# Performance work log

Hardware: AMD Instinct MI355X
Metric: run time of the kernel (lower is better)

## Reference

```python
import jax, jax.numpy as jnp
import numpy as np

C = 64       # channels per irrep
N = 50000    # nodes
E = 800000   # edges
A = 10       # node attribute (species) dim
R = 8        # radial basis features
H = 64       # radial MLP hidden width
INV3 = 1.0 / np.sqrt(3.0)  # CG norm for 1x1->0
INV2 = 1.0 / np.sqrt(2.0)  # CG norm for 1x1->1


def setup_inputs() -> dict:
    key = jax.random.key(0)
    ks = jax.random.split(key, 20)
    rn = lambda k, s, sc=1.0: jax.random.normal(k, s, dtype=jnp.float32) * sc
    sC = 1.0 / np.sqrt(C)
    inp = {}
    inp['node_features'] = rn(ks[0], (N, 4 * C))
    inp['node_attributes'] = jax.random.uniform(ks[1], (N, A), dtype=jnp.float32)
    inp['sph_harmonics'] = rn(ks[2], (E, 4))
    inp['radial_basis'] = jax.random.uniform(ks[3], (E, R), dtype=jnp.float32)
    inp['edge_index'] = jax.random.randint(ks[4], (2, E), 0, N)
    inp['pre_W0'] = rn(ks[5], (C, C), sC)
    inp['pre_W1'] = rn(ks[6], (C, C), sC)
    inp['mlp_W1'] = rn(ks[7], (R, H), 1.0 / np.sqrt(R))
    inp['mlp_W2'] = rn(ks[8], (H, H), 1.0 / np.sqrt(H))
    inp['mlp_W3'] = rn(ks[9], (H, 5 * C), 1.0 / np.sqrt(H))
    inp['lin0'] = rn(ks[10], (C, C), sC)
    inp['lin1'] = rn(ks[11], (C, C), sC)
    inp['c0_w'] = rn(ks[12], (A, 3, C), 1.0 / np.sqrt(A))
    inp['c1_w'] = rn(ks[13], (A, 2, C), 1.0 / np.sqrt(A))
    inp['sc_W0'] = rn(ks[14], (C, A, C), sC / np.sqrt(A))
    inp['sc_W1'] = rn(ks[15], (C, A, C), sC / np.sqrt(A))
    inp['fin0'] = rn(ks[16], (C, C), sC)
    inp['fin1'] = rn(ks[17], (C, C), sC)
    return inp


def reference(node_features, node_attributes, sph_harmonics, radial_basis,
              edge_index, pre_W0, pre_W1, mlp_W1, mlp_W2, mlp_W3, lin0, lin1,
              c0_w, c1_w, sc_W0, sc_W1, fin0, fin1):
    n = node_features.shape[0]
    # split flat features into irrep blocks: scalars (0e) and vectors (1o)
    x0 = node_features[:, :C]                        # [N, C]
    x1 = node_features[:, C:].reshape(n, C, 3)       # [N, C, 3]
    # --- interaction: pre linear (per-irrep channel mixing) ---
    h0 = x0 @ pre_W0
    h1 = jnp.einsum('ncm,cd->ndm', x1, pre_W1)
    snd, rcv = edge_index[0], edge_index[1]
    n0 = h0[snd]                                     # [E, C]
    n1 = h1[snd]                                     # [E, C, 3]
    y0 = sph_harmonics[:, :1]                        # [E, 1]
    y1 = sph_harmonics[:, 1:]                        # [E, 3]
    # radial MLP -> per-edge tensor-product path weights (SiLU, no bias)
    w = jax.nn.silu(radial_basis @ mlp_W1)
    w = jax.nn.silu(w @ mlp_W2)
    w = (w @ mlp_W3).reshape(-1, 5, C)               # [E, 5 paths, C]
    # Clebsch-Gordan tensor product paths (l<=1):
    #   0x0->0, 1x1->0, 0x1->1, 1x0->1, 1x1->1 (cross product)
    m0 = w[:, 0] * n0 * y0 + w[:, 1] * INV3 * jnp.einsum('ecm,em->ec', n1, y1)
    m1 = ((w[:, 2] * n0)[:, :, None] * y1[:, None, :]
          + w[:, 3][:, :, None] * n1 * y0[:, :, None]
          + w[:, 4][:, :, None] * INV2 * jnp.cross(n1, y1[:, None, :]))
    # neighbour aggregation: sum over receivers
    t0 = jax.ops.segment_sum(m0, rcv, num_segments=n)
    t1 = jax.ops.segment_sum(m1, rcv, num_segments=n)
    # post-interaction linear
    t0 = t0 @ lin0
    t1 = jnp.einsum('ncm,cd->ndm', t1, lin1)
    # --- symmetric contraction (correlation 2), attribute-dependent weights ---
    cw0 = jnp.einsum('na,apc->npc', node_attributes, c0_w)
    cw1 = jnp.einsum('na,apc->npc', node_attributes, c1_w)
    out0 = cw0[:, 0] * t0 + cw0[:, 1] * (t0 * t0) + cw0[:, 2] * jnp.sum(t1 * t1, axis=-1)
    out1 = cw1[:, 0][:, :, None] * t1 + cw1[:, 1][:, :, None] * (t0[:, :, None] * t1)
    # --- self-connection residual (fully connected TP with attrs 0e) ---
    out0 = out0 + jnp.einsum('nc,na,cad->nd', x0, node_attributes, sc_W0)
    out1 = out1 + jnp.einsum('ncm,na,cad->ndm', x1, node_attributes, sc_W1)
    # --- final linear ---
    f0 = out0 @ fin0
    f1 = jnp.einsum('ncm,cd->ndm', out1, fin1)
    return jnp.concatenate([f0, f1.reshape(n, 3 * C)], axis=-1)
```

## Files before the change

kernel.cpp:

```cpp
#include <hip/hip_runtime.h>
#include <hip/hip_bf16.h>
#include <cstdint>
#include <cstddef>

namespace {

constexpr int kN = 50000;
constexpr int kE = 800000;
constexpr int kPl = 3200000;
constexpr float kInv3 = 0.57735026918962576451f;
constexpr float kInv2 = 0.70710678118654752440f;

typedef __attribute__((ext_vector_type(8))) short bf16x8;
typedef __attribute__((ext_vector_type(4))) float f32x4;
union FragU { uint32_t u[4]; bf16x8 v; uint4 q; };

__device__ __forceinline__ float bcast(float v, int k) {
  return __int_as_float(__builtin_amdgcn_readlane(__float_as_int(v), k));
}
__device__ __forceinline__ int bcasti(int v, int k) {
  return __builtin_amdgcn_readlane(v, k);
}
__device__ __forceinline__ float silu(float x) {
  return x / (1.0f + __expf(-x));
}
__device__ __forceinline__ uint32_t bf16r(float f) {
  uint32_t u = __float_as_uint(f);
  return (u + 0x7fffu + ((u >> 16) & 1u)) >> 16;
}
__device__ __forceinline__ float blo(uint32_t u) { return __uint_as_float(u << 16); }
__device__ __forceinline__ float bhi(uint32_t u) { return __uint_as_float(u & 0xffff0000u); }
__device__ __forceinline__ uint32_t pk(float a, float b) {
  union { __hip_bfloat16 h; unsigned short s; } x, y;
  x.h = __float2bfloat16(a);
  y.h = __float2bfloat16(b);
  return (uint32_t)x.s | ((uint32_t)y.s << 16);
}

__global__ __launch_bounds__(256) void k_pre(const float* __restrict__ nf,
                                             const float* __restrict__ W0,
                                             const float* __restrict__ W1,
                                             float4* __restrict__ hcomb,
                                             unsigned short* __restrict__ xp) {
  __shared__ float sW[8192];
  __shared__ float sbuf[4][256];
  for (int i = threadIdx.x; i < 8192; i += 256)
    sW[i] = (i < 4096) ? W0[i] : W1[i - 4096];
  __syncthreads();

  const int wid = threadIdx.x >> 6, lane = threadIdx.x & 63;
  for (int nb = blockIdx.x * 4; nb < kN; nb += 2048 * 4) {
    const int n = nb + wid;
    if (n >= kN) continue;
    const float4 rv = ((const float4*)nf)[(size_t)n * 64 + lane];
    *(float4*)&sbuf[wid][lane * 4] = rv;
    const float v0 = sbuf[wid][lane];
    const float vx = sbuf[wid][64 + 3 * lane];
    const float vy = sbuf[wid][64 + 3 * lane + 1];
    const float vz = sbuf[wid][64 + 3 * lane + 2];
    xp[(size_t)n * 64 + lane] = (unsigned short)bf16r(vx);
    xp[(size_t)kPl + (size_t)n * 64 + lane] = (unsigned short)bf16r(vy);
    xp[(size_t)2 * kPl + (size_t)n * 64 + lane] = (unsigned short)bf16r(vz);
    float a0 = 0.f, ax = 0.f, ay = 0.f, az = 0.f;
#pragma unroll
    for (int k = 0; k < 64; ++k) {
      const float w0 = sW[k * 64 + lane];
      const float w1 = sW[4096 + k * 64 + lane];
      a0 = fmaf(bcast(v0, k), w0, a0);
      ax = fmaf(bcast(vx, k), w1, ax);
      ay = fmaf(bcast(vy, k), w1, ay);
      az = fmaf(bcast(vz, k), w1, az);
    }
    hcomb[(size_t)n * 64 + lane] = make_float4(a0, ax, ay, az);
  }
}

__global__ void k_hist(const int* __restrict__ ei, int* __restrict__ cnt) {
  const int e = blockIdx.x * blockDim.x + threadIdx.x;
  if (e < kE) atomicAdd(&cnt[ei[kE + e]], 1);
}

__global__ __launch_bounds__(1024) void k_scan(const int* __restrict__ cnt,
                                               int* __restrict__ starts) {
  __shared__ int sh[1024];
  const int t = threadIdx.x;
  constexpr int CH = 49;
  const int base = t * CH;
  int s = 0;
  for (int i = 0; i < CH; ++i) {
    const int idx = base + i;
    if (idx < kN) s += cnt[idx];
  }
  sh[t] = s;
  __syncthreads();
  for (int off = 1; off < 1024; off <<= 1) {
    const int v = sh[t];
    const int o = (t >= off) ? sh[t - off] : 0;
    __syncthreads();
    sh[t] = v + o;
    __syncthreads();
  }
  int run = sh[t] - s;
  for (int i = 0; i < CH; ++i) {
    const int idx = base + i;
    if (idx < kN) {
      starts[idx] = run;
      run += cnt[idx];
    }
  }
}

__global__ void k_scatter(const int* __restrict__ ei, int* __restrict__ cursor,
                          int* __restrict__ eids) {
  const int e = blockIdx.x * blockDim.x + threadIdx.x;
  if (e < kE) {
    const int pos = atomicAdd(&cursor[ei[kE + e]], 1);
    eids[pos] = e;
  }
}

__device__ __forceinline__ void xpose(const uint32_t* pa, const uint32_t* pb,
                                      int addr0, int addr1, bool ghi,
                                      FragU* out) {
#pragma unroll
  for (int kt = 0; kt < 2; ++kt) {
    const int m0 = 2 * kt, m1 = 2 * kt + 1;
    int t0, t1;
    t0 = __builtin_amdgcn_ds_bpermute(addr0, (int)pa[m0]);
    t1 = __builtin_amdgcn_ds_bpermute(addr0, (int)pa[m1]);
    out[kt].u[0] = (uint32_t)(ghi ? t1 : t0);
    t0 = __builtin_amdgcn_ds_bpermute(addr0, (int)pb[m0]);
    t1 = __builtin_amdgcn_ds_bpermute(addr0, (int)pb[m1]);
    out[kt].u[1] = (uint32_t)(ghi ? t1 : t0);
    t0 = __builtin_amdgcn_ds_bpermute(addr1, (int)pa[m0]);
    t1 = __builtin_amdgcn_ds_bpermute(addr1, (int)pa[m1]);
    out[kt].u[2] = (uint32_t)(ghi ? t1 : t0);
    t0 = __builtin_amdgcn_ds_bpermute(addr1, (int)pb[m0]);
    t1 = __builtin_amdgcn_ds_bpermute(addr1, (int)pb[m1]);
    out[kt].u[3] = (uint32_t)(ghi ? t1 : t0);
  }
}

__global__ __launch_bounds__(256, 2) void k_mlp(
    const float* __restrict__ rb, const int* __restrict__ eids,
    const float* __restrict__ W1f, const float* __restrict__ W2f,
    const float* __restrict__ W3f, uint32_t* __restrict__ wout,
    int tile0, int ntiles) {
  __shared__ uint32_t sfrag[13312];
  for (int i = threadIdx.x; i < 13312; i += 256) {
    const int f = i >> 8, l = (i >> 2) & 63, jp = i & 3;
    const int kk = ((l >> 4) << 3) + 2 * jp;
    float a, b;
    if (f < 4) {
      const int c = (f << 4) + (l & 15);
      a = (kk < 8) ? W1f[kk * 64 + c] : 0.f;
      b = (kk < 7) ? W1f[(kk + 1) * 64 + c] : 0.f;
    } else if (f < 12) {
      const int kt = (f - 4) >> 2, mt = (f - 4) & 3;
      const int k = kt * 32 + kk, c = (mt << 4) + (l & 15);
      a = W2f[k * 64 + c];
      b = W2f[(k + 1) * 64 + c];
    } else {
      const int kt = (f - 12) / 20, mt = (f - 12) % 20;
      const int k = kt * 32 + kk, c = (mt << 4) + (l & 15);
      a = W3f[k * 320 + c];
      b = W3f[(k + 1) * 320 + c];
    }
    sfrag[i] = pk(a, b);
  }
  __syncthreads();

  const int lane = threadIdx.x & 63;
  const int e15 = lane & 15, g = lane >> 4;
  const uint4* fr = (const uint4*)sfrag;
  const int wv = blockIdx.x * 4 + (threadIdx.x >> 6);
  const int addr0 = ((((g & 1) << 1)) * 16 + e15) * 4;
  const int addr1 = addr0 + 64;
  const bool ghi = (g >> 1) != 0;
  const f32x4 z = {0.f, 0.f, 0.f, 0.f};

  for (int t = wv; t < ntiles; t += 768 * 4) {
    FragU b1;
    b1.u[0] = b1.u[1] = b1.u[2] = b1.u[3] = 0;
    if (lane < 16) {
      const int e = eids[(size_t)(tile0 + t) * 16 + lane];
      const float4 r0 = *(const float4*)(rb + (size_t)e * 8);
      const float4 r1 = *(const float4*)(rb + (size_t)e * 8 + 4);
      b1.u[0] = pk(r0.x, r0.y);
      b1.u[1] = pk(r0.z, r0.w);
      b1.u[2] = pk(r1.x, r1.y);
      b1.u[3] = pk(r1.z, r1.w);
    }

    uint32_t pa[4], pb[4];
#pragma unroll
    for (int mt = 0; mt < 4; ++mt) {
      FragU a;
      a.q = fr[(mt << 6) + lane];
      f32x4 d = __builtin_amdgcn_mfma_f32_16x16x32_bf16(a.v, b1.v, z, 0, 0, 0);
      pa[mt] = pk(silu(d[0]), silu(d[1]));
      pb[mt] = pk(silu(d[2]), silu(d[3]));
    }
    FragU b2[2];
    xpose(pa, pb, addr0, addr1, ghi, b2);

    f32x4 d2[4] = {z, z, z, z};
#pragma unroll
    for (int kt = 0; kt < 2; ++kt)
#pragma unroll
      for (int mt = 0; mt < 4; ++mt) {
        FragU a;
        a.q = fr[((4 + kt * 4 + mt) << 6) + lane];
        d2[mt] =
            __builtin_amdgcn_mfma_f32_16x16x32_bf16(a.v, b2[kt].v, d2[mt], 0, 0, 0);
      }
#pragma unroll
    for (int mt = 0; mt < 4; ++mt) {
      pa[mt] = pk(silu(d2[mt][0]), silu(d2[mt][1]));
      pb[mt] = pk(silu(d2[mt][2]), silu(d2[mt][3]));
    }
    FragU b3[2];
    xpose(pa, pb, addr0, addr1, ghi, b3);

    uint32_t* wt = wout + (size_t)t * 2560 + lane;
#pragma unroll 4
    for (int mt = 0; mt < 20; ++mt) {
      FragU a0, a1;
      a0.q = fr[((12 + mt) << 6) + lane];
      a1.q = fr[((32 + mt) << 6) + lane];
      f32x4 d = __builtin_amdgcn_mfma_f32_16x16x32_bf16(a0.v, b3[0].v, z, 0, 0, 0);
      d = __builtin_amdgcn_mfma_f32_16x16x32_bf16(a1.v, b3[1].v, d, 0, 0, 0);
      wt[mt * 128] = pk(d[0], d[1]);
      wt[mt * 128 + 64] = pk(d[2], d[3]);
    }
  }
}

__global__ __launch_bounds__(1024, 6) void k_edge2(
    const float* __restrict__ sph, const int* __restrict__ ei,
    const int* __restrict__ eids, const int* __restrict__ ends,
    const int* __restrict__ cnts, const uint32_t* __restrict__ w32,
    const float4* __restrict__ hcomb, float4* __restrict__ tcomb,
    int lo, int hi) {
  const int lane = threadIdx.x & 63;
  const int LCb = ((lane >> 4) << 7) + (((lane & 3) >> 1) << 6) +
                  (((lane >> 2) & 3) << 4);
  const uint32_t shl = (lane & 1) ? 0u : 16u;
  const int gw = blockIdx.x * 16 + (threadIdx.x >> 6);
  for (int n = gw; n < kN; n += 512 * 16) {
    int tmp = 0;
    if (lane == 0) tmp = ends[n];
    else if (lane == 1) tmp = cnts[n];
    const int end = bcasti(tmp, 0);
    const int cn = bcasti(tmp, 1);
    const int s0 = max(end - cn, lo);
    const int s1 = min(end, hi);
    if (s0 >= s1) continue;
    float a0 = 0.f, axx = 0.f, ayy = 0.f, azz = 0.f;

    for (int base = s0; base < s1; base += 64) {
      const int m = min(64, s1 - base);
      int sidv = 0;
      float4 svv = make_float4(0.f, 0.f, 0.f, 0.f);
      if (lane < m) {
        const int ev = eids[base + lane];
        sidv = ei[ev];
        svv = *(const float4*)(sph + (size_t)ev * 4);
      }
      const int scur = bcasti(sidv, 0);
      float4 h = hcomb[(size_t)scur * 64 + lane];
      const int sl0 = base - lo;
      size_t wi = (size_t)(sl0 >> 4) * 2560 + (sl0 & 15) + LCb;
      uint32_t u0 = w32[wi], u1 = w32[wi + 512], u2 = w32[wi + 1024],
               u3 = w32[wi + 1536], u4 = w32[wi + 2048];

      for (int j = 0; j < m; ++j) {
        float4 hn = h;
        uint32_t n0 = u0, n1 = u1, n2 = u2, n3 = u3, n4 = u4;
        if (j + 1 < m) {
          const int sn = bcasti(sidv, j + 1);
          hn = hcomb[(size_t)sn * 64 + lane];
          const int sl = base + j + 1 - lo;
          const size_t wj = (size_t)(sl >> 4) * 2560 + (sl & 15) + LCb;
          n0 = w32[wj];
          n1 = w32[wj + 512];
          n2 = w32[wj + 1024];
          n3 = w32[wj + 1536];
          n4 = w32[wj + 2048];
        }
        const float y0 = bcast(svv.x, j), y1 = bcast(svv.y, j);
        const float y2 = bcast(svv.z, j), y3 = bcast(svv.w, j);
        const float w0 = __uint_as_float((u0 << shl) & 0xffff0000u);
        const float w1v = __uint_as_float((u1 << shl) & 0xffff0000u);
        const float w2v = __uint_as_float((u2 << shl) & 0xffff0000u);
        const float w3v = __uint_as_float((u3 << shl) & 0xffff0000u);
        const float w4v = __uint_as_float((u4 << shl) & 0xffff0000u);

        const float dot = h.y * y1 + h.z * y2 + h.w * y3;
        const float m0 = w0 * h.x * y0 + w1v * kInv3 * dot;
        const float cx = h.z * y3 - h.w * y2;
        const float cy = h.w * y1 - h.y * y3;
        const float cz = h.y * y2 - h.z * y1;
        const float t2 = w2v * h.x;
        const float c4 = w4v * kInv2;
        const float w3y0 = w3v * y0;
        a0 += m0;
        axx += t2 * y1 + w3y0 * h.y + c4 * cx;
        ayy += t2 * y2 + w3y0 * h.z + c4 * cy;
        azz += t2 * y3 + w3y0 * h.w + c4 * cz;
        h = hn;
        u0 = n0; u1 = n1; u2 = n2; u3 = n3; u4 = n4;
      }
    }
    const size_t idx = (size_t)n * 64 + lane;
    float4 t = tcomb[idx];
    t.x += a0; t.y += axx; t.z += ayy; t.w += azz;
    tcomb[idx] = t;
  }
}

__global__ __launch_bounds__(512, 4) void k_edge(
    const float* __restrict__ rb, const float* __restrict__ sph,
    const int* __restrict__ ei, const int* __restrict__ eids,
    const int* __restrict__ ends, const int* __restrict__ cnts,
    const float* __restrict__ W1, const float* __restrict__ W2,
    const float* __restrict__ W3, const float4* __restrict__ hcomb,
    float4* __restrict__ tcomb) {
  extern __shared__ float sm[];
  uint32_t* smu = (uint32_t*)sm;
  for (int i = threadIdx.x; i < 12800; i += 512) {
    if (i < 512) {
      sm[i] = W1[i];
    } else if (i < 2560) {
      const int j = i - 512;
      const int c = j >> 5, kp = j & 31;
      const int dst = 512 + c * 32 + (((kp >> 2) ^ (c & 7)) << 2) + (kp & 3);
      smu[dst] = bf16r(W2[(2 * kp) * 64 + c]) |
                 (bf16r(W2[(2 * kp + 1) * 64 + c]) << 16);
    } else {
      const int j = i - 2560;
      const int q = j >> 11, r = j & 2047;
      const int c = r >> 5, kp = r & 31;
      const int dst =
          2560 + q * 2048 + c * 32 + (((kp >> 2) ^ (c & 7)) << 2) + (kp & 3);
      smu[dst] = bf16r(W3[(2 * kp) * 320 + q * 64 + c]) |
                 (bf16r(W3[(2 * kp + 1) * 320 + q * 64 + c]) << 16);
    }
  }
  __syncthreads();

  const float* sW1 = sm;
  const uint32_t* sW2p = smu + 512;
  const uint32_t* sW3p = smu + 2560;
  const int lane = threadIdx.x & 63;
  const int gw = blockIdx.x * 8 + (threadIdx.x >> 6);
  const int rowoff = lane * 32;
  const int lsw = lane & 7;

  for (int n = gw; n < kN; n += 1024 * 8) {
    int tmp = 0;
    if (lane == 0) tmp = ends[n];
    else if (lane == 1) tmp = cnts[n];
    const int end = bcasti(tmp, 0);
    const int cn = bcasti(tmp, 1);
    float a0 = 0.f, axx = 0.f, ayy = 0.f, azz = 0.f;

    for (int base = end - cn; base < end; base += 64) {
      const int m = min(64, end - base);
      int sidv = 0;
      float4 r0v = make_float4(0.f, 0.f, 0.f, 0.f);
      float4 r1v = r0v, svv = r0v;
      if (lane < m) {
        const int e = eids[base + lane];
        sidv = ei[e];
        r0v = *(const float4*)(rb + (size_t)e * 8);
        r1v = *(const float4*)(rb + (size_t)e * 8 + 4);
        svv = *(const float4*)(sph + (size_t)e * 4);
      }
      const int sid0 = bcasti(sidv, 0);
      float4 h = hcomb[(size_t)sid0 * 64 + lane];

      for (int j = 0; j < m; ++j) {
        float4 hn = h;
        if (j + 1 < m) {
          const int sn = bcasti(sidv, j + 1);
          hn = hcomb[(size_t)sn * 64 + lane];
        }
        const float e0 = bcast(r0v.x, j), e1 = bcast(r0v.y, j);
        const float e2 = bcast(r0v.z, j), e3 = bcast(r0v.w, j);
        const float e4 = bcast(r1v.x, j), e5 = bcast(r1v.y, j);
        const float e6 = bcast(r1v.z, j), e7 = bcast(r1v.w, j);
        const float y0 = bcast(svv.x, j), y1 = bcast(svv.y, j);
        const float y2 = bcast(svv.z, j), y3 = bcast(svv.w, j);

        float acc = e0 * sW1[lane];
        acc = fmaf(e1, sW1[64 + lane], acc);
        acc = fmaf(e2, sW1[128 + lane], acc);
        acc = fmaf(e3, sW1[192 + lane], acc);
        acc = fmaf(e4, sW1[256 + lane], acc);
        acc = fmaf(e5, sW1[320 + lane], acc);
        acc = fmaf(e6, sW1[384 + lane], acc);
        acc = fmaf(e7, sW1[448 + lane], acc);
        const float h1 = silu(acc);

        float acc2 = 0.f;
#pragma unroll
        for (int k8 = 0; k8 < 8; ++k8) {
          const uint4 w = *(const uint4*)(sW2p + rowoff + ((k8 ^ lsw) << 2));
          acc2 = fmaf(bcast(h1, 8 * k8 + 0), blo(w.x), acc2);
          acc2 = fmaf(bcast(h1, 8 * k8 + 1), bhi(w.x), acc2);
          acc2 = fmaf(bcast(h1, 8 * k8 + 2), blo(w.y), acc2);
          acc2 = fmaf(bcast(h1, 8 * k8 + 3), bhi(w.y), acc2);
          acc2 = fmaf(bcast(h1, 8 * k8 + 4), blo(w.z), acc2);
          acc2 = fmaf(bcast(h1, 8 * k8 + 5), bhi(w.z), acc2);
          acc2 = fmaf(bcast(h1, 8 * k8 + 6), blo(w.w), acc2);
          acc2 = fmaf(bcast(h1, 8 * k8 + 7), bhi(w.w), acc2);
        }
        const float h2 = silu(acc2);

        float w0 = 0.f, w1v = 0.f, w2v = 0.f, w3v = 0.f, w4v = 0.f;
#pragma unroll 2
        for (int k8 = 0; k8 < 8; ++k8) {
          const int off = rowoff + ((k8 ^ lsw) << 2);
          const uint4 p0 = *(const uint4*)(sW3p + off);
          const uint4 p1 = *(const uint4*)(sW3p + 2048 + off);
          const uint4 p2 = *(const uint4*)(sW3p + 4096 + off);
          const uint4 p3 = *(const uint4*)(sW3p + 6144 + off);
          const uint4 p4 = *(const uint4*)(sW3p + 8192 + off);
          const float k0 = bcast(h2, 8 * k8 + 0);
          const float k1 = bcast(h2, 8 * k8 + 1);
          const float k2 = bcast(h2, 8 * k8 + 2);
          const float k3 = bcast(h2, 8 * k8 + 3);
          const float k4 = bcast(h2, 8 * k8 + 4);
          const float k5 = bcast(h2, 8 * k8 + 5);
          const float k6 = bcast(h2, 8 * k8 + 6);
          const float k7 = bcast(h2, 8 * k8 + 7);
          w0 = fmaf(k0, blo(p0.x), w0); w0 = fmaf(k1, bhi(p0.x), w0);
          w0 = fmaf(k2, blo(p0.y), w0); w0 = fmaf(k3, bhi(p0.y), w0);
          w0 = fmaf(k4, blo(p0.z), w0); w0 = fmaf(k5, bhi(p0.z), w0);
          w0 = fmaf(k6, blo(p0.w), w0); w0 = fmaf(k7, bhi(p0.w), w0);
          w1v = fmaf(k0, blo(p1.x), w1v); w1v = fmaf(k1, bhi(p1.x), w1v);
          w1v = fmaf(k2, blo(p1.y), w1v); w1v = fmaf(k3, bhi(p1.y), w1v);
          w1v = fmaf(k4, blo(p1.z), w1v); w1v = fmaf(k5, bhi(p1.z), w1v);
          w1v = fmaf(k6, blo(p1.w), w1v); w1v = fmaf(k7, bhi(p1.w), w1v);
          w2v = fmaf(k0, blo(p2.x), w2v); w2v = fmaf(k1, bhi(p2.x), w2v);
          w2v = fmaf(k2, blo(p2.y), w2v); w2v = fmaf(k3, bhi(p2.y), w2v);
          w2v = fmaf(k4, blo(p2.z), w2v); w2v = fmaf(k5, bhi(p2.z), w2v);
          w2v = fmaf(k6, blo(p2.w), w2v); w2v = fmaf(k7, bhi(p2.w), w2v);
          w3v = fmaf(k0, blo(p3.x), w3v); w3v = fmaf(k1, bhi(p3.x), w3v);
          w3v = fmaf(k2, blo(p3.y), w3v); w3v = fmaf(k3, bhi(p3.y), w3v);
          w3v = fmaf(k4, blo(p3.z), w3v); w3v = fmaf(k5, bhi(p3.z), w3v);
          w3v = fmaf(k6, blo(p3.w), w3v); w3v = fmaf(k7, bhi(p3.w), w3v);
          w4v = fmaf(k0, blo(p4.x), w4v); w4v = fmaf(k1, bhi(p4.x), w4v);
          w4v = fmaf(k2, blo(p4.y), w4v); w4v = fmaf(k3, bhi(p4.y), w4v);
          w4v = fmaf(k4, blo(p4.z), w4v); w4v = fmaf(k5, bhi(p4.z), w4v);
          w4v = fmaf(k6, blo(p4.w), w4v); w4v = fmaf(k7, bhi(p4.w), w4v);
        }

        const float dot = h.y * y1 + h.z * y2 + h.w * y3;
        const float m0 = w0 * h.x * y0 + w1v * kInv3 * dot;
        const float cx = h.z * y3 - h.w * y2;
        const float cy = h.w * y1 - h.y * y3;
        const float cz = h.y * y2 - h.z * y1;
        const float t2 = w2v * h.x;
        const float c4 = w4v * kInv2;
        const float w3y0 = w3v * y0;
        a0 += m0;
        axx += t2 * y1 + w3y0 * h.y + c4 * cx;
        ayy += t2 * y2 + w3y0 * h.z + c4 * cy;
        azz += t2 * y3 + w3y0 * h.w + c4 * cz;
        h = hn;
      }
    }
    tcomb[(size_t)n * 64 + lane] = make_float4(a0, axx, ayy, azz);
  }
}

__global__ __launch_bounds__(1024, 2) void k_sc2(
    const float* __restrict__ nf, const float* __restrict__ attrs,
    const unsigned short* __restrict__ xp, const float* __restrict__ scW0,
    const float* __restrict__ scW1, float* __restrict__ scout) {
  extern __shared__ uint32_t sfr[];
  const int lane = threadIdx.x & 63, wid = threadIdx.x >> 6;
  const int tile = blockIdx.x * 16 + wid;
  const bool act = (tile < kN / 16);
  const int node = lane & 15, g = lane >> 4;
  const int n = tile * 16 + node;
  const uint4* fr = (const uint4*)sfr;
  const f32x4 z4 = {0.f, 0.f, 0.f, 0.f};

  float at[10];
#pragma unroll
  for (int a = 0; a < 10; ++a)
    at[a] = act ? attrs[(size_t)n * 10 + a] : 0.f;

  for (int i = threadIdx.x; i < 20480; i += 1024) {
    const int f = i >> 8, l = (i >> 2) & 63, jp = i & 3;
    const int kt = f >> 2, mt = f & 3;
    const int c = mt * 16 + (l & 15);
    const int kl = ((l >> 4) << 3) + 2 * jp;
    const int k = ((kt & 1) << 5) + kl, a = kt >> 1;
    sfr[i] = pk(scW0[(size_t)k * 640 + a * 64 + c],
                scW0[(size_t)(k + 1) * 640 + a * 64 + c]);
  }
  __syncthreads();
  if (act) {
    uint32_t x0u[2][4];
#pragma unroll
    for (int kh = 0; kh < 2; ++kh) {
      const float4 v0 = *(const float4*)(nf + (size_t)n * 256 + kh * 32 + g * 8);
      const float4 v1 =
          *(const float4*)(nf + (size_t)n * 256 + kh * 32 + g * 8 + 4);
      x0u[kh][0] = pk(v0.x, v0.y);
      x0u[kh][1] = pk(v0.z, v0.w);
      x0u[kh][2] = pk(v1.x, v1.y);
      x0u[kh][3] = pk(v1.z, v1.w);
    }
    f32x4 acc[4] = {z4, z4, z4, z4};
#pragma unroll 2
    for (int kt = 0; kt < 20; ++kt) {
      const float av = at[kt >> 1];
      const int kh = kt & 1;
      FragU b;
#pragma unroll
      for (int i = 0; i < 4; ++i)
        b.u[i] = pk(av * blo(x0u[kh][i]), av * bhi(x0u[kh][i]));
#pragma unroll
      for (int mt = 0; mt < 4; ++mt) {
        FragU a;
        a.q = fr[(kt * 4 + mt) * 64 + lane];
        acc[mt] = __builtin_amdgcn_mfma_f32_16x16x32_bf16(a.v, b.v, acc[mt],
                                                          0, 0, 0);
      }
    }
#pragma unroll
    for (int mt = 0; mt < 4; ++mt)
#pragma unroll
      for (int r = 0; r < 4; ++r)
        scout[(size_t)n * 64 + mt * 16 + g * 4 + r] = acc[mt][r];
  }
  __syncthreads();

  for (int i = threadIdx.x; i < 20480; i += 1024) {
    const int f = i >> 8, l = (i >> 2) & 63, jp = i & 3;
    const int kt = f >> 2, mt = f & 3;
    const int c = mt * 16 + (l & 15);
    const int kl = ((l >> 4) << 3) + 2 * jp;
    const int k = ((kt & 1) << 5) + kl, a = kt >> 1;
    sfr[i] = pk(scW1[(size_t)k * 640 + a * 64 + c],
                scW1[(size_t)(k + 1) * 640 + a * 64 + c]);
  }
  __syncthreads();
  if (act) {
    uint32_t x1u[3][2][4];
#pragma unroll
    for (int m = 0; m < 3; ++m)
#pragma unroll
      for (int kh = 0; kh < 2; ++kh) {
        const uint4 v = *(const uint4*)(xp + (size_t)m * kPl + (size_t)n * 64 +
                                        kh * 32 + g * 8);
        x1u[m][kh][0] = v.x;
        x1u[m][kh][1] = v.y;
        x1u[m][kh][2] = v.z;
        x1u[m][kh][3] = v.w;
      }
    f32x4 acc[3][4] = {{z4, z4, z4, z4}, {z4, z4, z4, z4}, {z4, z4, z4, z4}};
#pragma unroll 2
    for (int kt = 0; kt < 20; ++kt) {
      const float av = at[kt >> 1];
      const int kh = kt & 1;
      FragU b[3];
#pragma unroll
      for (int m = 0; m < 3; ++m)
#pragma unroll
        for (int i = 0; i < 4; ++i)
          b[m].u[i] = pk(av * blo(x1u[m][kh][i]), av * bhi(x1u[m][kh][i]));
#pragma unroll
      for (int mt = 0; mt < 4; ++mt) {
        FragU a;
        a.q = fr[(kt * 4 + mt) * 64 + lane];
#pragma unroll
        for (int m = 0; m < 3; ++m)
          acc[m][mt] = __builtin_amdgcn_mfma_f32_16x16x32_bf16(
              a.v, b[m].v, acc[m][mt], 0, 0, 0);
      }
    }
#pragma unroll
    for (int m = 0; m < 3; ++m)
#pragma unroll
      for (int mt = 0; mt < 4; ++mt)
#pragma unroll
        for (int r = 0; r < 4; ++r)
          scout[(size_t)(m + 1) * kPl + (size_t)n * 64 + mt * 16 + g * 4 + r] =
              acc[m][mt][r];
  }
}

__global__ __launch_bounds__(1024, 1) void k_post(
    const float* __restrict__ attrs,
    const float* __restrict__ lin0, const float* __restrict__ lin1,
    const float* __restrict__ c0w, const float* __restrict__ c1w,
    const float* __restrict__ fin0, const float* __restrict__ fin1,
    const float4* __restrict__ tcomb, const float* __restrict__ scout,
    float4* __restrict__ out) {
  extern __shared__ float sm[];
  float* sl0 = sm;
  float* sl1 = sm + 4096;
  float* sf0 = sm + 8192;
  float* sf1 = sm + 12288;
  __shared__ float sc0[1920];
  __shared__ float sc1[1280];
  for (int i = threadIdx.x; i < 4096; i += 1024) {
    sl0[i] = lin0[i];
    sl1[i] = lin1[i];
    sf0[i] = fin0[i];
    sf1[i] = fin1[i];
  }
  for (int i = threadIdx.x; i < 1920; i += 1024) sc0[i] = c0w[i];
  for (int i = threadIdx.x; i < 1280; i += 1024) sc1[i] = c1w[i];
  __syncthreads();

  const int lane = threadIdx.x & 63;
  float* sb = sm + 16384 + (threadIdx.x >> 6) * 256;
  for (int n = blockIdx.x * 16 + (threadIdx.x >> 6); n < kN; n += 512 * 16) {
    const float4 t = tcomb[(size_t)n * 64 + lane];
    float avl = 0.f;
    if (lane < 10) avl = attrs[(size_t)n * 10 + lane];
    float b0 = 0.f, bx = 0.f, by = 0.f, bz = 0.f;
#pragma unroll
    for (int k = 0; k < 64; ++k) {
      const float w0 = sl0[k * 64 + lane];
      const float w1 = sl1[k * 64 + lane];
      b0 = fmaf(bcast(t.x, k), w0, b0);
      bx = fmaf(bcast(t.y, k), w1, bx);
      by = fmaf(bcast(t.z, k), w1, by);
      bz = fmaf(bcast(t.w, k), w1, bz);
    }
    float cw00 = 0.f, cw01 = 0.f, cw02 = 0.f, cw10 = 0.f, cw11 = 0.f;
#pragma unroll
    for (int a = 0; a < 10; ++a) {
      const float av = bcast(avl, a);
      cw00 = fmaf(av, sc0[a * 192 + lane], cw00);
      cw01 = fmaf(av, sc0[a * 192 + 64 + lane], cw01);
      cw02 = fmaf(av, sc0[a * 192 + 128 + lane], cw02);
      cw10 = fmaf(av, sc1[a * 128 + lane], cw10);
      cw11 = fmaf(av, sc1[a * 128 + 64 + lane], cw11);
    }
    const size_t pidx = (size_t)n * 64 + lane;
    const float scx = scout[pidx];
    const float scy = scout[(size_t)kPl + pidx];
    const float scz = scout[(size_t)2 * kPl + pidx];
    const float scw = scout[(size_t)3 * kPl + pidx];
    const float o0 = cw00 * b0 + cw01 * b0 * b0 +
                     cw02 * (bx * bx + by * by + bz * bz) + scx;
    const float o1x = cw10 * bx + cw11 * b0 * bx + scy;
    const float o1y = cw10 * by + cw11 * b0 * by + scz;
    const float o1z = cw10 * bz + cw11 * b0 * bz + scw;
    float f0 = 0.f, fx = 0.f, fy = 0.f, fz = 0.f;
#pragma unroll
    for (int k = 0; k < 64; ++k) {
      const float w0 = sf0[k * 64 + lane];
      const float w1 = sf1[k * 64 + lane];
      f0 = fmaf(bcast(o0, k), w0, f0);
      fx = fmaf(bcast(o1x, k), w1, fx);
      fy = fmaf(bcast(o1y, k), w1, fy);
      fz = fmaf(bcast(o1z, k), w1, fz);
    }
    sb[lane] = f0;
    sb[64 + 3 * lane] = fx;
    sb[64 + 3 * lane + 1] = fy;
    sb[64 + 3 * lane + 2] = fz;
    out[(size_t)n * 64 + lane] = *(const float4*)&sb[lane * 4];
  }
}

}

extern "C" void kernel_launch(void* const* d_in, const int* in_sizes, int n_in,
                              void* d_out, int out_size, void* d_ws,
                              size_t ws_size, hipStream_t stream) {
  (void)in_sizes; (void)n_in; (void)out_size;
  const float* nf = (const float*)d_in[0];
  const float* attrs = (const float*)d_in[1];
  const float* sph = (const float*)d_in[2];
  const float* rb = (const float*)d_in[3];
  const int* ei = (const int*)d_in[4];
  const float* preW0 = (const float*)d_in[5];
  const float* preW1 = (const float*)d_in[6];
  const float* mW1 = (const float*)d_in[7];
  const float* mW2 = (const float*)d_in[8];
  const float* mW3 = (const float*)d_in[9];
  const float* lin0 = (const float*)d_in[10];
  const float* lin1 = (const float*)d_in[11];
  const float* c0w = (const float*)d_in[12];
  const float* c1w = (const float*)d_in[13];
  const float* scW0 = (const float*)d_in[14];
  const float* scW1 = (const float*)d_in[15];
  const float* fin0 = (const float*)d_in[16];
  const float* fin1 = (const float*)d_in[17];
  float4* out = (float4*)d_out;

  char* ws = (char*)d_ws;
  float4* hcomb = (float4*)ws;
  float4* tcomb = (float4*)(ws + 51200000);
  int* cnts = (int*)(ws + 102400000);
  int* starts = (int*)(ws + 102600000);
  int* eids = (int*)(ws + 102800000);
  unsigned short* xp = (unsigned short*)(ws + 106000000);
  uint32_t* wbuf = (uint32_t*)(ws + 125200000);
  float* scout = (float*)hcomb;

  long long avail = (long long)ws_size - 125200000ll;
  long long cs64 = (avail > 0) ? avail / 640 : 0;
  if (cs64 > kE) cs64 = kE;
  const int chunkSlots = (int)(cs64 & ~15ll);
  const bool mfma = (chunkSlots >= 64000);

  hipMemsetAsync(cnts, 0, kN * sizeof(int), stream);
  k_pre<<<2048, 256, 0, stream>>>(nf, preW0, preW1, hcomb, xp);
  k_hist<<<(kE + 255) / 256, 256, 0, stream>>>(ei, cnts);
  k_scan<<<1, 1024, 0, stream>>>(cnts, starts);
  k_scatter<<<(kE + 255) / 256, 256, 0, stream>>>(ei, starts, eids);

  if (mfma) {
    hipMemsetAsync(tcomb, 0, (size_t)kN * 1024, stream);
    int done = 0;
    while (done < kE) {
      const int cs = (kE - done < chunkSlots) ? (kE - done) : chunkSlots;
      const int tiles = cs / 16;
      k_mlp<<<768, 256, 0, stream>>>(rb, eids, mW1, mW2, mW3, wbuf,
                                     done / 16, tiles);
      k_edge2<<<512, 1024, 0, stream>>>(sph, ei, eids, starts, cnts, wbuf,
                                        hcomb, tcomb, done, done + cs);
      done += cs;
    }
  } else {
    hipFuncSetAttribute((const void*)k_edge,
                        hipFuncAttributeMaxDynamicSharedMemorySize, 12800 * 4);
    k_edge<<<1024, 512, 12800 * 4, stream>>>(rb, sph, ei, eids, starts, cnts,
                                             mW1, mW2, mW3, hcomb, tcomb);
  }

  hipFuncSetAttribute((const void*)k_sc2,
                      hipFuncAttributeMaxDynamicSharedMemorySize, 81920);
  k_sc2<<<196, 1024, 81920, stream>>>(nf, attrs, xp, scW0, scW1, scout);

  hipFuncSetAttribute((const void*)k_post,
                      hipFuncAttributeMaxDynamicSharedMemorySize, 20480 * 4);
  k_post<<<512, 1024, 20480 * 4, stream>>>(attrs, lin0, lin1, c0w, c1w,
                                           fin0, fin1, tcomb, scout, out);
}
```

Measured before the change: 1.160 ms.

## Deepen edge-loop prefetch to double-buffered groups of four edges

Replaces the one-edge-ahead software prefetch in the per-node edge aggregation loop with ping-pong buffers of four edges each. Loads for the next group are issued while the current group is computed, so more gather loads of node features and bf16 edge weights are in flight. This raises register use, so launch bounds drop from 6 to 4 waves per SIMD, trading occupancy for memory-level parallelism per wave.

```diff
diff --git a/kernel.cpp b/kernel.cpp
--- a/kernel.cpp
+++ b/kernel.cpp
@@ -236,7 +236,54 @@
   }
 }
 
-__global__ __launch_bounds__(1024, 6) void k_edge2(
+#define LOAD_GRP(WH, HH, JG)                                               \
+  {                                                                        \
+    _Pragma("unroll") for (int jj = 0; jj < 4; ++jj) {                     \
+      const int j = (JG) + jj;                                             \
+      if (j < m) {                                                         \
+        const int sn = bcasti(sidv, j);                                    \
+        HH[jj] = hcomb[(size_t)sn * 64 + lane];                            \
+        const int sl = base + j - lo;                                      \
+        const size_t wj = (size_t)(sl >> 4) * 2560 + (sl & 15) + LCb;      \
+        WH[jj][0] = w32[wj];                                               \
+        WH[jj][1] = w32[wj + 512];                                         \
+        WH[jj][2] = w32[wj + 1024];                                        \
+        WH[jj][3] = w32[wj + 1536];                                        \
+        WH[jj][4] = w32[wj + 2048];                                        \
+      }                                                                    \
+    }                                                                      \
+  }
+
+#define COMP_GRP(WH, HH, JG)                                               \
+  {                                                                        \
+    _Pragma("unroll") for (int jj = 0; jj < 4; ++jj) {                     \
+      const int j = (JG) + jj;                                             \
+      if (j < m) {                                                         \
+        const float y0 = bcast(svv.x, j), y1 = bcast(svv.y, j);            \
+        const float y2 = bcast(svv.z, j), y3 = bcast(svv.w, j);            \
+        const float4 h = HH[jj];                                           \
+        const float w0 = __uint_as_float((WH[jj][0] << shl) & 0xffff0000u);\
+        const float w1v = __uint_as_float((WH[jj][1] << shl) & 0xffff0000u);\
+        const float w2v = __uint_as_float((WH[jj][2] << shl) & 0xffff0000u);\
+        const float w3v = __uint_as_float((WH[jj][3] << shl) & 0xffff0000u);\
+        const float w4v = __uint_as_float((WH[jj][4] << shl) & 0xffff0000u);\
+        const float dot = h.y * y1 + h.z * y2 + h.w * y3;                  \
+        const float m0 = w0 * h.x * y0 + w1v * kInv3 * dot;                \
+        const float cx = h.z * y3 - h.w * y2;                              \
+        const float cy = h.w * y1 - h.y * y3;                              \
+        const float cz = h.y * y2 - h.z * y1;                              \
+        const float t2 = w2v * h.x;                                        \
+        const float c4 = w4v * kInv2;                                      \
+        const float w3y0 = w3v * y0;                                       \
+        a0 += m0;                                                          \
+        axx += t2 * y1 + w3y0 * h.y + c4 * cx;                             \
+        ayy += t2 * y2 + w3y0 * h.z + c4 * cy;                             \
+        azz += t2 * y3 + w3y0 * h.w + c4 * cz;                             \
+      }                                                                    \
+    }                                                                      \
+  }
+
+__global__ __launch_bounds__(1024, 4) void k_edge2(
     const float* __restrict__ sph, const int* __restrict__ ei,
     const int* __restrict__ eids, const int* __restrict__ ends,
     const int* __restrict__ cnts, const uint32_t* __restrict__ w32,
@@ -267,49 +314,15 @@
         sidv = ei[ev];
         svv = *(const float4*)(sph + (size_t)ev * 4);
       }
-      const int scur = bcasti(sidv, 0);
-      float4 h = hcomb[(size_t)scur * 64 + lane];
-      const int sl0 = base - lo;
-      size_t wi = (size_t)(sl0 >> 4) * 2560 + (sl0 & 15) + LCb;
-      uint32_t u0 = w32[wi], u1 = w32[wi + 512], u2 = w32[wi + 1024],
-               u3 = w32[wi + 1536], u4 = w32[wi + 2048];
-
-      for (int j = 0; j < m; ++j) {
-        float4 hn = h;
-        uint32_t n0 = u0, n1 = u1, n2 = u2, n3 = u3, n4 = u4;
-        if (j + 1 < m) {
-          const int sn = bcasti(sidv, j + 1);
-          hn = hcomb[(size_t)sn * 64 + lane];
-          const int sl = base + j + 1 - lo;
-          const size_t wj = (size_t)(sl >> 4) * 2560 + (sl & 15) + LCb;
-          n0 = w32[wj];
-          n1 = w32[wj + 512];
-          n2 = w32[wj + 1024];
-          n3 = w32[wj + 1536];
-          n4 = w32[wj + 2048];
-        }
-        const float y0 = bcast(svv.x, j), y1 = bcast(svv.y, j);
-        const float y2 = bcast(svv.z, j), y3 = bcast(svv.w, j);
-        const float w0 = __uint_as_float((u0 << shl) & 0xffff0000u);
-        const float w1v = __uint_as_float((u1 << shl) & 0xffff0000u);
-        const float w2v = __uint_as_float((u2 << shl) & 0xffff0000u);
-        const float w3v = __uint_as_float((u3 << shl) & 0xffff0000u);
-        const float w4v = __uint_as_float((u4 << shl) & 0xffff0000u);
-
-        const float dot = h.y * y1 + h.z * y2 + h.w * y3;
-        const float m0 = w0 * h.x * y0 + w1v * kInv3 * dot;
-        const float cx = h.z * y3 - h.w * y2;
-        const float cy = h.w * y1 - h.y * y3;
-        const float cz = h.y * y2 - h.z * y1;
-        const float t2 = w2v * h.x;
-        const float c4 = w4v * kInv2;
-        const float w3y0 = w3v * y0;
-        a0 += m0;
-        axx += t2 * y1 + w3y0 * h.y + c4 * cx;
-        ayy += t2 * y2 + w3y0 * h.z + c4 * cy;
-        azz += t2 * y3 + w3y0 * h.w + c4 * cz;
-        h = hn;
-        u0 = n0; u1 = n1; u2 = n2; u3 = n3; u4 = n4;
+
+      uint32_t wA[4][5], wB[4][5];
+      float4 hA[4], hB[4];
+      LOAD_GRP(wA, hA, 0);
+      for (int jg = 0; jg < m; jg += 8) {
+        LOAD_GRP(wB, hB, jg + 4);
+        COMP_GRP(wA, hA, jg);
+        LOAD_GRP(wA, hA, jg + 8);
+        COMP_GRP(wB, hB, jg + 4);
       }
     }
     const size_t idx = (size_t)n * 64 + lane;
@@ -318,6 +331,9 @@
     tcomb[idx] = t;
   }
 }
+
+#undef LOAD_GRP
+#undef COMP_GRP
 
 __global__ __launch_bounds__(512, 4) void k_edge(
     const float* __restrict__ rb, const float* __restrict__ sph,
```

After: 1.177 ms. Within noise of the previous version (+1.5%).
